# Optimization experiments

Measured on AMD Instinct MI355X. Metric: run time of the kernel, lower is better.

## Reference

```python
import jax, jax.numpy as jnp
import numpy as np

LEAKY_SLOPE = 0.01  # torch nn.LeakyReLU / F.leaky_relu default


def gcn_diffusion(adj, order, feat):
    # A_gcn = adj + I; sym-normalized diffusion D^-1/2 A D^-1/2 applied repeatedly
    B, N, _ = adj.shape
    A = adj + jnp.eye(N, dtype=adj.dtype)
    dinv_sqrt = jnp.sum(A, axis=2) ** -0.5  # [B, N]
    outs = []
    h = feat
    for _ in range(order):
        h = jnp.matmul(A, dinv_sqrt[..., None] * h) * dinv_sqrt[..., None]
        outs.append(h)
    return outs


def scattering_s4(adj, feat):
    # lazy random walk P = 1/2 (I + A D^-1); wavelets Psi_j = P^{2^{j-1}} - P^{2^j}
    dinv = 1.0 / jnp.sum(adj, axis=2)  # [B, N]
    p = feat
    us = []
    for _ in range(8):  # powers P^1 .. P^8
        p = 0.5 * p + 0.5 * jnp.matmul(adj, dinv[..., None] * p)
        us.append(p)
    h1 = feat - us[0]      # I - P
    h2 = us[0] - us[1]     # P - P^2
    h3 = us[1] - us[3]     # P^2 - P^4
    h4 = us[3] - us[7]     # P^4 - P^8
    return h1, h2, h3, h4


def sctconv(X, adj, W1, b1, W2, b2, a, moment):
    leaky = lambda x: jax.nn.leaky_relu(x, LEAKY_SLOPE)
    h = X  # [B, N, F]
    hA, hA2, hA3 = gcn_diffusion(adj, 3, X)
    hA, hA2, hA3 = leaky(hA), leaky(hA2), leaky(hA3)
    s1, s2, s3, s4 = scattering_s4(adj, X)
    mom = jnp.asarray(moment, dtype=X.dtype)
    s1 = jnp.abs(s1) ** mom
    s2 = jnp.abs(s2) ** mom
    s3 = jnp.abs(s3) ** mom
    s4 = jnp.abs(s4) ** mom
    # NOTE: original concatenates only (hA, hA2, s1..s4) -> 6 branches; hA3 is unused.
    h_all = jnp.stack([hA, hA2, s1, s2, s3, s4], axis=1)  # [B, 6, N, F]
    h_b = jnp.broadcast_to(h[:, None], h_all.shape)        # [B, 6, N, F]
    a_input = jnp.concatenate([h_b, h_all], axis=3)        # [B, 6, N, 2F]
    e = jnp.einsum('bknc,c->bkn', jax.nn.relu(a_input), a[:, 0])  # [B, 6, N]
    attention = jax.nn.softmax(e, axis=1)[..., None]       # [B, 6, N, 1]
    h_prime = jnp.mean(attention * h_all, axis=1)          # [B, N, F]
    out = leaky(h_prime @ W1.T + b1)
    out = leaky(out @ W2.T + b2)
    return out


def setup_inputs() -> dict:
    key = jax.random.key(0)
    kx, ka, k1, k2, k3, k4, k5 = jax.random.split(key, 7)
    B, N, F = 8, 4096, 64
    X = jax.random.normal(kx, (B, N, F), dtype=jnp.float32)
    adj = jax.random.uniform(ka, (B, N, N), dtype=jnp.float32)
    s = 1.0 / np.sqrt(F)
    W1 = jax.random.uniform(k1, (F, F), minval=-s, maxval=s, dtype=jnp.float32)
    b1 = jax.random.uniform(k2, (F,), minval=-s, maxval=s, dtype=jnp.float32)
    W2 = jax.random.uniform(k3, (F, F), minval=-s, maxval=s, dtype=jnp.float32)
    b2 = jax.random.uniform(k4, (F,), minval=-s, maxval=s, dtype=jnp.float32)
    a = jax.random.normal(k5, (2 * F, 1), dtype=jnp.float32) * 0.1
    return {"X": X, "adj": adj, "W1": W1, "b1": b1, "W2": W2, "b2": b2, "a": a, "moment": 1}


def reference(X, adj, W1, b1, W2, b2, a, moment):
    return sctconv(X, adj, W1, b1, W2, b2, a, moment)
```

## Files before the change

### kernel.cpp

```cpp
#include <hip/hip_runtime.h>
#include <hip/hip_bf16.h>
#include <cstdio>
#include <cstdint>

#define BB 8
#define NN 4096
#define FF 64

typedef __attribute__((ext_vector_type(8))) short bf16x8;
typedef __attribute__((ext_vector_type(4))) float f32x4;

__device__ __forceinline__ unsigned short f2bf(float f){
  unsigned int u = __float_as_uint(f);
  u += 0x7FFFu + ((u >> 16) & 1u);
  return (unsigned short)(u >> 16);
}

__device__ __forceinline__ float leaky01(float x){ return x > 0.f ? x : 0.01f * x; }

__global__ __launch_bounds__(256) void k_convert(const float* __restrict__ adj,
    unsigned short* __restrict__ adjb, float* __restrict__ dinv, float* __restrict__ dsq)
{
  size_t row = blockIdx.x;
  const float4* src = (const float4*)(adj + row * NN);
  ushort4* dst = (ushort4*)(adjb + row * NN);
  float s = 0.f;
  for (int i = threadIdx.x; i < NN / 4; i += 256){
    float4 v = src[i];
    s += (v.x + v.y) + (v.z + v.w);
    dst[i] = make_ushort4(f2bf(v.x), f2bf(v.y), f2bf(v.z), f2bf(v.w));
  }
  for (int o = 32; o; o >>= 1) s += __shfl_xor(s, o);
  __shared__ float red[4];
  if ((threadIdx.x & 63) == 0) red[threadIdx.x >> 6] = s;
  __syncthreads();
  if (threadIdx.x == 0){
    float t = (red[0] + red[1]) + (red[2] + red[3]);
    dinv[row] = 1.0f / t;
    dsq[row]  = 1.0f / sqrtf(t + 1.0f);
  }
}

__global__ __launch_bounds__(256) void k_prep(const float* __restrict__ X,
    const float* __restrict__ dinv, const float* __restrict__ dsq,
    unsigned short* __restrict__ vt)
{
  const int b = blockIdx.y, n0 = blockIdx.x * 64, tid = threadIdx.x;
  __shared__ unsigned short tg[64][65], ts[64][65];
  #pragma unroll
  for (int i = 0; i < 4; ++i){
    int idx = i * 256 + tid, n = idx >> 4, c4 = (idx & 15) * 4;
    size_t rb = (size_t)b * NN + n0 + n;
    float4 x = *(const float4*)(X + rb * 64 + c4);
    float di = dinv[b * NN + n0 + n], dv = dsq[b * NN + n0 + n];
    tg[c4 + 0][n] = f2bf(dv * x.x); tg[c4 + 1][n] = f2bf(dv * x.y);
    tg[c4 + 2][n] = f2bf(dv * x.z); tg[c4 + 3][n] = f2bf(dv * x.w);
    ts[c4 + 0][n] = f2bf(di * x.x); ts[c4 + 1][n] = f2bf(di * x.y);
    ts[c4 + 2][n] = f2bf(di * x.z); ts[c4 + 3][n] = f2bf(di * x.w);
  }
  __syncthreads();
  #pragma unroll
  for (int i = 0; i < 4; ++i){
    int idx = i * 256 + tid, c = idx >> 4, n4 = (idx & 15) * 4;
    *(ushort4*)(vt + ((size_t)b * 128 + c) * NN + n0 + n4) =
        make_ushort4(tg[c][n4], tg[c][n4 + 1], tg[c][n4 + 2], tg[c][n4 + 3]);
    *(ushort4*)(vt + ((size_t)b * 128 + 64 + c) * NN + n0 + n4) =
        make_ushort4(ts[c][n4], ts[c][n4 + 1], ts[c][n4 + 2], ts[c][n4 + 3]);
  }
}

template<int NC>
__global__ __launch_bounds__(256, 4) void k_gemm_fused(
    const unsigned short* __restrict__ adjb,
    const unsigned short* __restrict__ vtR, int c0,
    const float* __restrict__ sprev, float* __restrict__ P, float* __restrict__ snap,
    const float* __restrict__ dinv, int writeVtS,
    const float* __restrict__ gprev, float* __restrict__ gout,
    const float* __restrict__ dsq, int writeVtG,
    unsigned short* __restrict__ vtW)
{
  constexpr int NF = NC / 64;
  constexpr int BI = NC / 32;
  __shared__ __align__(16) unsigned short As[2][32 * 64];
  __shared__ __align__(16) unsigned short Bs[2][NC * 64];
  const int b = blockIdx.y;
  const int m0 = blockIdx.x * 32;
  const int tid = threadIdx.x;
  const int w = tid >> 6, l = tid & 63;
  const unsigned short* Ag = adjb + (size_t)b * NN * NN;
  const unsigned short* Bg = vtR + ((size_t)b * 128 + c0) * NN;

  auto stage = [&](int buf, int k0){
    {
      int r = tid >> 3, g = tid & 7;
      const unsigned short* gp = Ag + (size_t)(m0 + r) * NN + k0 + ((g ^ (r & 7)) << 3);
      __builtin_amdgcn_global_load_lds((const __attribute__((address_space(1))) void*)gp,
          (__attribute__((address_space(3))) void*)(&As[buf][tid << 3]), 16, 0, 0);
    }
    #pragma unroll
    for (int i = 0; i < BI; ++i){
      int idx = i * 256 + tid, c = idx >> 3, g = idx & 7;
      const unsigned short* gp = Bg + (size_t)c * NN + k0 + ((g ^ (c & 7)) << 3);
      __builtin_amdgcn_global_load_lds((const __attribute__((address_space(1))) void*)gp,
          (__attribute__((address_space(3))) void*)(&Bs[buf][idx << 3]), 16, 0, 0);
    }
  };

  f32x4 acc[2][NF];
  #pragma unroll
  for (int mi = 0; mi < 2; ++mi)
    #pragma unroll
    for (int ni = 0; ni < NF; ++ni)
      #pragma unroll
      for (int j = 0; j < 4; ++j) acc[mi][ni][j] = 0.f;

  stage(0, 0);
  const int r0 = l & 15, hq = l >> 4, sw = r0 & 7;
  constexpr int NT = NN / 64;
  for (int t = 0; t < NT; ++t){
    const int cur = t & 1;
    if (t + 1 < NT){
      stage(cur ^ 1, (t + 1) * 64);
      if constexpr (NC == 128) asm volatile("s_waitcnt vmcnt(5)" ::: "memory");
      else                     asm volatile("s_waitcnt vmcnt(3)" ::: "memory");
    } else {
      asm volatile("s_waitcnt vmcnt(0)" ::: "memory");
    }
    __builtin_amdgcn_s_barrier();
    asm volatile("" ::: "memory");
    #pragma unroll
    for (int kk = 0; kk < 2; ++kk){
      const int g8 = ((kk * 4 + hq) ^ sw) << 3;
      bf16x8 af[2], bfr[NF];
      #pragma unroll
      for (int mi = 0; mi < 2; ++mi)
        af[mi] = *(const bf16x8*)&As[cur][(mi * 16 + r0) * 64 + g8];
      #pragma unroll
      for (int ni = 0; ni < NF; ++ni)
        bfr[ni] = *(const bf16x8*)&Bs[cur][(w * 16 * NF + ni * 16 + r0) * 64 + g8];
      #pragma unroll
      for (int mi = 0; mi < 2; ++mi)
        #pragma unroll
        for (int ni = 0; ni < NF; ++ni)
          acc[mi][ni] = __builtin_amdgcn_mfma_f32_16x16x32_bf16(af[mi], bfr[ni], acc[mi][ni], 0, 0, 0);
    }
    asm volatile("" ::: "memory");
    __builtin_amdgcn_s_barrier();
    asm volatile("" ::: "memory");
  }

  const bool isScat = (NC == 64) || (w >= 2);
  if (isScat){
    const int wS = (NC == 64) ? w : (w - 2);
    #pragma unroll
    for (int mi = 0; mi < 2; ++mi){
      const int rb = m0 + mi * 16 + hq * 4;
      const size_t rowb = (size_t)b * NN + rb;
      float4 dv4 = *(const float4*)(dinv + (size_t)b * NN + rb);
      #pragma unroll
      for (int ni = 0; ni < NF; ++ni){
        const int cs = wS * 16 * NF + ni * 16 + r0;
        float pn[4];
        #pragma unroll
        for (int j = 0; j < 4; ++j){
          float pv = sprev[(rowb + j) * 64 + cs];
          pn[j] = 0.5f * (pv + acc[mi][ni][j]);
          P[(rowb + j) * 64 + cs] = pn[j];
        }
        if (snap){
          #pragma unroll
          for (int j = 0; j < 4; ++j) snap[(rowb + j) * 64 + cs] = pn[j];
        }
        if (writeVtS){
          ushort4 vv = make_ushort4(f2bf(dv4.x * pn[0]), f2bf(dv4.y * pn[1]),
                                    f2bf(dv4.z * pn[2]), f2bf(dv4.w * pn[3]));
          *(ushort4*)(vtW + ((size_t)b * 128 + 64 + cs) * NN + rb) = vv;
        }
      }
    }
  }
  if constexpr (NC == 128){
    if (!isScat){
      #pragma unroll
      for (int mi = 0; mi < 2; ++mi){
        const int rb = m0 + mi * 16 + hq * 4;
        const size_t rowb = (size_t)b * NN + rb;
        float4 dq4 = *(const float4*)(dsq + (size_t)b * NN + rb);
        #pragma unroll
        for (int ni = 0; ni < NF; ++ni){
          const int cg = w * 16 * NF + ni * 16 + r0;
          float hn[4];
          const float dq[4] = {dq4.x, dq4.y, dq4.z, dq4.w};
          #pragma unroll
          for (int j = 0; j < 4; ++j){
            float hv = gprev[(rowb + j) * 64 + cg];
            hn[j] = (acc[mi][ni][j] + dq[j] * hv) * dq[j];
            gout[(rowb + j) * 64 + cg] = hn[j];
          }
          if (writeVtG){
            ushort4 vv = make_ushort4(f2bf(dq[0] * hn[0]), f2bf(dq[1] * hn[1]),
                                      f2bf(dq[2] * hn[2]), f2bf(dq[3] * hn[3]));
            *(ushort4*)(vtW + ((size_t)b * 128 + cg) * NN + rb) = vv;
          }
        }
      }
    }
  }
}

__global__ __launch_bounds__(256) void k_attn(
    const float* __restrict__ X,  const float* __restrict__ hA, const float* __restrict__ hA2,
    const float* __restrict__ U1, const float* __restrict__ U2, const float* __restrict__ U4,
    const float* __restrict__ U8, const float* __restrict__ W1, const float* __restrict__ b1,
    const float* __restrict__ W2, const float* __restrict__ b2, const float* __restrict__ av,
    const int* __restrict__ momp, float* __restrict__ out)
{
  __shared__ float W1s[64][65], W2s[64][65];
  __shared__ float a1s[64], a2s[64], b1s[64], b2s[64];
  __shared__ float hp[4][64], o1[4][64];
  const int tid = threadIdx.x;
  for (int e = tid; e < 4096; e += 256){
    W1s[e >> 6][e & 63] = W1[e];
    W2s[e >> 6][e & 63] = W2[e];
  }
  if (tid < 64){ a1s[tid] = av[tid]; a2s[tid] = av[64 + tid]; b1s[tid] = b1[tid]; b2s[tid] = b2[tid]; }
  __syncthreads();
  const int w = tid >> 6, l = tid & 63;
  size_t row = (size_t)blockIdx.x * 4 + w;
  size_t off = row * 64 + l;
  float x  = X[off];
  float u1 = U1[off], u2 = U2[off], u4 = U4[off], u8 = U8[off];
  float br[6];
  br[0] = leaky01(hA[off]);
  br[1] = leaky01(hA2[off]);
  float d1 = fabsf(x - u1), d2 = fabsf(u1 - u2), d3 = fabsf(u2 - u4), d4 = fabsf(u4 - u8);
  int mom = *momp;
  if (mom == 1){ br[2] = d1; br[3] = d2; br[4] = d3; br[5] = d4; }
  else {
    float m = (float)mom;
    br[2] = powf(d1, m); br[3] = powf(d2, m); br[4] = powf(d3, m); br[5] = powf(d4, m);
  }
  float v = fmaxf(x, 0.f) * a1s[l];
  for (int o = 32; o; o >>= 1) v += __shfl_xor(v, o);
  float base = v;
  float e[6];
  #pragma unroll
  for (int k = 0; k < 6; ++k){
    float t = fmaxf(br[k], 0.f) * a2s[l];
    for (int o = 32; o; o >>= 1) t += __shfl_xor(t, o);
    e[k] = base + t;
  }
  float mx = e[0];
  #pragma unroll
  for (int k = 1; k < 6; ++k) mx = fmaxf(mx, e[k]);
  float s = 0.f, att[6];
  #pragma unroll
  for (int k = 0; k < 6; ++k){ att[k] = expf(e[k] - mx); s += att[k]; }
  float inv = 1.0f / (6.0f * s);
  float hpv = 0.f;
  #pragma unroll
  for (int k = 0; k < 6; ++k) hpv += att[k] * br[k];
  hpv *= inv;
  hp[w][l] = hpv;
  __syncthreads();
  float acc = b1s[l];
  #pragma unroll 8
  for (int c = 0; c < 64; ++c) acc += hp[w][c] * W1s[l][c];
  o1[w][l] = leaky01(acc);
  __syncthreads();
  float acc2 = b2s[l];
  #pragma unroll 8
  for (int c = 0; c < 64; ++c) acc2 += o1[w][c] * W2s[l][c];
  out[off] = leaky01(acc2);
}

static constexpr size_t OFF_ADJB = 0;
static constexpr size_t OFF_VTA  = OFF_ADJB + (size_t)BB * NN * NN * 2;
static constexpr size_t OFF_VTB  = OFF_VTA  + (size_t)BB * 128 * NN * 2;
static constexpr size_t OFF_HA   = OFF_VTB  + (size_t)BB * 128 * NN * 2;
static constexpr size_t OFF_HA2  = OFF_HA   + (size_t)BB * NN * 64 * 4;
static constexpr size_t OFF_P    = OFF_HA2  + (size_t)BB * NN * 64 * 4;
static constexpr size_t OFF_U1   = OFF_P    + (size_t)BB * NN * 64 * 4;
static constexpr size_t OFF_U2   = OFF_U1   + (size_t)BB * NN * 64 * 4;
static constexpr size_t OFF_U4   = OFF_U2   + (size_t)BB * NN * 64 * 4;
static constexpr size_t OFF_U8   = OFF_U4   + (size_t)BB * NN * 64 * 4;
static constexpr size_t OFF_DINV = OFF_U8   + (size_t)BB * NN * 64 * 4;
static constexpr size_t OFF_DS   = OFF_DINV + (size_t)BB * NN * 4;
static constexpr size_t WS_NEED  = OFF_DS   + (size_t)BB * NN * 4;

extern "C" void kernel_launch(void* const* d_in, const int* in_sizes, int n_in,
                              void* d_out, int out_size, void* d_ws, size_t ws_size,
                              hipStream_t stream)
{
  const float* X   = (const float*)d_in[0];
  const float* adj = (const float*)d_in[1];
  const float* W1  = (const float*)d_in[2];
  const float* b1  = (const float*)d_in[3];
  const float* W2  = (const float*)d_in[4];
  const float* b2  = (const float*)d_in[5];
  const float* av  = (const float*)d_in[6];
  const int*  momp = (const int*)d_in[7];
  float* out = (float*)d_out;

  if (ws_size < WS_NEED){
    fprintf(stderr, "kernel_launch: workspace too small: %zu < %zu\n", ws_size, WS_NEED);
    return;
  }
  char* w = (char*)d_ws;
  unsigned short* adjb = (unsigned short*)(w + OFF_ADJB);
  unsigned short* vtA  = (unsigned short*)(w + OFF_VTA);
  unsigned short* vtB  = (unsigned short*)(w + OFF_VTB);
  float* hA   = (float*)(w + OFF_HA);
  float* hA2  = (float*)(w + OFF_HA2);
  float* P    = (float*)(w + OFF_P);
  float* U1   = (float*)(w + OFF_U1);
  float* U2   = (float*)(w + OFF_U2);
  float* U4   = (float*)(w + OFF_U4);
  float* U8   = (float*)(w + OFF_U8);
  float* dinv = (float*)(w + OFF_DINV);
  float* dsq  = (float*)(w + OFF_DS);

  k_convert<<<BB * NN, 256, 0, stream>>>(adj, adjb, dinv, dsq);
  dim3 tg64(NN / 64, BB);
  k_prep<<<tg64, 256, 0, stream>>>(X, dinv, dsq, vtA);

  dim3 gg(NN / 32, BB);
  k_gemm_fused<128><<<gg, 256, 0, stream>>>(adjb, vtA, 0,
      X, P, U1, dinv, 1, X, hA, dsq, 1, vtB);
  k_gemm_fused<128><<<gg, 256, 0, stream>>>(adjb, vtB, 0,
      P, P, U2, dinv, 1, hA, hA2, dsq, 0, vtA);
  unsigned short* vr = vtA;
  unsigned short* vw = vtB;
  for (int k = 3; k <= 8; ++k){
    float* snap = (k == 4) ? U4 : (k == 8) ? nullptr : nullptr;
    float* pdst = (k == 8) ? U8 : P;
    if (k == 4) snap = U4;
    k_gemm_fused<64><<<gg, 256, 0, stream>>>(adjb, vr, 64,
        P, pdst, snap, dinv, (k < 8) ? 1 : 0, nullptr, nullptr, nullptr, 0, vw);
    unsigned short* t = vr; vr = vw; vw = t;
  }

  k_attn<<<BB * NN / 4, 256, 0, stream>>>(X, hA, hA2, U1, U2, U4, U8,
                                          W1, b1, W2, b2, av, momp, out);
}
```

Measured before the change: 832.6 us.

## Pre-tile bf16 adjacency into swizzled contiguous blocks and interleave batches across blocks

The conversion kernel now writes the bf16 adjacency in a pre-tiled, pre-swizzled layout, so each 32x64 A tile the GEMM stages is one contiguous 4 KB chunk rather than 32 strided row segments. The GEMM grid is flattened so consecutive blocks cycle through batches (b = bid & 7), which changes the order in which blocks touch the L2/MALL. The conversion's row-sum reduction is reworked to match the new tiling, using an 8-lane shuffle in place of a block-wide reduction. The intent is better DRAM and cache locality for the eight repeated adjacency sweeps, at the cost of a more complex layout coupling the two kernels.

```diff
diff --git a/kernel.cpp b/kernel.cpp
--- a/kernel.cpp
+++ b/kernel.cpp
@@ -19,25 +19,29 @@
 __device__ __forceinline__ float leaky01(float x){ return x > 0.f ? x : 0.01f * x; }
 
 __global__ __launch_bounds__(256) void k_convert(const float* __restrict__ adj,
-    unsigned short* __restrict__ adjb, float* __restrict__ dinv, float* __restrict__ dsq)
-{
-  size_t row = blockIdx.x;
-  const float4* src = (const float4*)(adj + row * NN);
-  ushort4* dst = (ushort4*)(adjb + row * NN);
+    unsigned short* __restrict__ At, float* __restrict__ dinv, float* __restrict__ dsq)
+{
+  const int bid = blockIdx.x;
+  const int b = bid & 7, mt = bid >> 3, m0 = mt * 32;
+  const int tid = threadIdx.x;
+  const int r = tid >> 3, g = tid & 7;
+  const float* src = adj + ((size_t)b * NN + m0 + r) * NN + ((g ^ (r & 7)) << 3);
+  unsigned short* dst = At + (size_t)bid * 64 * 2048 + (tid << 3);
   float s = 0.f;
-  for (int i = threadIdx.x; i < NN / 4; i += 256){
-    float4 v = src[i];
-    s += (v.x + v.y) + (v.z + v.w);
-    dst[i] = make_ushort4(f2bf(v.x), f2bf(v.y), f2bf(v.z), f2bf(v.w));
-  }
-  for (int o = 32; o; o >>= 1) s += __shfl_xor(s, o);
-  __shared__ float red[4];
-  if ((threadIdx.x & 63) == 0) red[threadIdx.x >> 6] = s;
-  __syncthreads();
-  if (threadIdx.x == 0){
-    float t = (red[0] + red[1]) + (red[2] + red[3]);
-    dinv[row] = 1.0f / t;
-    dsq[row]  = 1.0f / sqrtf(t + 1.0f);
+  for (int t = 0; t < 64; ++t){
+    const float* p = src + t * 64;
+    float4 a = *(const float4*)p;
+    float4 c = *(const float4*)(p + 4);
+    s += ((a.x + a.y) + (a.z + a.w)) + ((c.x + c.y) + (c.z + c.w));
+    bf16x8 v;
+    v[0] = (short)f2bf(a.x); v[1] = (short)f2bf(a.y); v[2] = (short)f2bf(a.z); v[3] = (short)f2bf(a.w);
+    v[4] = (short)f2bf(c.x); v[5] = (short)f2bf(c.y); v[6] = (short)f2bf(c.z); v[7] = (short)f2bf(c.w);
+    *(bf16x8*)(dst + (size_t)t * 2048) = v;
+  }
+  s += __shfl_xor(s, 1); s += __shfl_xor(s, 2); s += __shfl_xor(s, 4);
+  if (g == 0){
+    dinv[(size_t)b * NN + m0 + r] = 1.0f / s;
+    dsq [(size_t)b * NN + m0 + r] = 1.0f / sqrtf(s + 1.0f);
   }
 }
 
@@ -71,7 +75,7 @@
 
 template<int NC>
 __global__ __launch_bounds__(256, 4) void k_gemm_fused(
-    const unsigned short* __restrict__ adjb,
+    const unsigned short* __restrict__ At,
     const unsigned short* __restrict__ vtR, int c0,
     const float* __restrict__ sprev, float* __restrict__ P, float* __restrict__ snap,
     const float* __restrict__ dinv, int writeVtS,
@@ -83,24 +87,23 @@
   constexpr int BI = NC / 32;
   __shared__ __align__(16) unsigned short As[2][32 * 64];
   __shared__ __align__(16) unsigned short Bs[2][NC * 64];
-  const int b = blockIdx.y;
-  const int m0 = blockIdx.x * 32;
+  const int bid = blockIdx.x;
+  const int b = bid & 7, mt = bid >> 3, m0 = mt * 32;
   const int tid = threadIdx.x;
   const int w = tid >> 6, l = tid & 63;
-  const unsigned short* Ag = adjb + (size_t)b * NN * NN;
+  const unsigned short* Atile = At + (size_t)bid * 64 * 2048;
   const unsigned short* Bg = vtR + ((size_t)b * 128 + c0) * NN;
 
-  auto stage = [&](int buf, int k0){
+  auto stage = [&](int buf, int t){
     {
-      int r = tid >> 3, g = tid & 7;
-      const unsigned short* gp = Ag + (size_t)(m0 + r) * NN + k0 + ((g ^ (r & 7)) << 3);
+      const unsigned short* gp = Atile + (size_t)t * 2048 + (tid << 3);
       __builtin_amdgcn_global_load_lds((const __attribute__((address_space(1))) void*)gp,
           (__attribute__((address_space(3))) void*)(&As[buf][tid << 3]), 16, 0, 0);
     }
     #pragma unroll
     for (int i = 0; i < BI; ++i){
       int idx = i * 256 + tid, c = idx >> 3, g = idx & 7;
-      const unsigned short* gp = Bg + (size_t)c * NN + k0 + ((g ^ (c & 7)) << 3);
+      const unsigned short* gp = Bg + (size_t)c * NN + t * 64 + ((g ^ (c & 7)) << 3);
       __builtin_amdgcn_global_load_lds((const __attribute__((address_space(1))) void*)gp,
           (__attribute__((address_space(3))) void*)(&Bs[buf][idx << 3]), 16, 0, 0);
     }
@@ -120,7 +123,7 @@
   for (int t = 0; t < NT; ++t){
     const int cur = t & 1;
     if (t + 1 < NT){
-      stage(cur ^ 1, (t + 1) * 64);
+      stage(cur ^ 1, t + 1);
       if constexpr (NC == 128) asm volatile("s_waitcnt vmcnt(5)" ::: "memory");
       else                     asm volatile("s_waitcnt vmcnt(3)" ::: "memory");
     } else {
@@ -307,9 +310,9 @@
     return;
   }
   char* w = (char*)d_ws;
-  unsigned short* adjb = (unsigned short*)(w + OFF_ADJB);
-  unsigned short* vtA  = (unsigned short*)(w + OFF_VTA);
-  unsigned short* vtB  = (unsigned short*)(w + OFF_VTB);
+  unsigned short* At  = (unsigned short*)(w + OFF_ADJB);
+  unsigned short* vtA = (unsigned short*)(w + OFF_VTA);
+  unsigned short* vtB = (unsigned short*)(w + OFF_VTB);
   float* hA   = (float*)(w + OFF_HA);
   float* hA2  = (float*)(w + OFF_HA2);
   float* P    = (float*)(w + OFF_P);
@@ -320,22 +323,20 @@
   float* dinv = (float*)(w + OFF_DINV);
   float* dsq  = (float*)(w + OFF_DS);
 
-  k_convert<<<BB * NN, 256, 0, stream>>>(adj, adjb, dinv, dsq);
+  k_convert<<<1024, 256, 0, stream>>>(adj, At, dinv, dsq);
   dim3 tg64(NN / 64, BB);
   k_prep<<<tg64, 256, 0, stream>>>(X, dinv, dsq, vtA);
 
-  dim3 gg(NN / 32, BB);
-  k_gemm_fused<128><<<gg, 256, 0, stream>>>(adjb, vtA, 0,
+  k_gemm_fused<128><<<1024, 256, 0, stream>>>(At, vtA, 0,
       X, P, U1, dinv, 1, X, hA, dsq, 1, vtB);
-  k_gemm_fused<128><<<gg, 256, 0, stream>>>(adjb, vtB, 0,
+  k_gemm_fused<128><<<1024, 256, 0, stream>>>(At, vtB, 0,
       P, P, U2, dinv, 1, hA, hA2, dsq, 0, vtA);
   unsigned short* vr = vtA;
   unsigned short* vw = vtB;
   for (int k = 3; k <= 8; ++k){
-    float* snap = (k == 4) ? U4 : (k == 8) ? nullptr : nullptr;
+    float* snap = (k == 4) ? U4 : nullptr;
     float* pdst = (k == 8) ? U8 : P;
-    if (k == 4) snap = U4;
-    k_gemm_fused<64><<<gg, 256, 0, stream>>>(adjb, vr, 64,
+    k_gemm_fused<64><<<1024, 256, 0, stream>>>(At, vr, 64,
         P, pdst, snap, dinv, (k < 8) ? 1 : 0, nullptr, nullptr, nullptr, 0, vw);
     unsigned short* t = vr; vr = vw; vw = t;
   }
```

Result: faster. 772.9 us (-7.2%).
